# Optimization experiments

Hardware: AMD Instinct MI355X
Metric: run time of the kernel (lower is better)

## Reference

```python
import jax, jax.numpy as jnp
import numpy as np

N = 50000      # num nodes
E = 800000     # num edges (avg degree 16)
D = 128        # feature dim
HOP = 2        # number of propagation hops
FILL = 0.5     # self-loop fill value (A_hat = A + fill*I)


def setup_inputs() -> dict:
    key = jax.random.key(0)
    k1, k2, k3, k4, k5 = jax.random.split(key, 5)
    x_s = jax.random.normal(k1, (N, D), dtype=jnp.float32)
    x_t = jax.random.normal(k2, (N, D), dtype=jnp.float32)
    src = jax.random.randint(k3, (E,), 0, N)
    # guarantee no pre-existing self-loops so that appending all self-loops
    # exactly matches add_remaining_self_loops
    dst = (src + jax.random.randint(k4, (E,), 1, N)) % N
    edge_index = jnp.stack([src, dst]).astype(jnp.int32)
    edge_weight = jax.random.uniform(k5, (E,), dtype=jnp.float32)
    # DIMPA parameters, initialized to 1.0 per _reset_parameters
    w_s = jnp.ones((HOP + 1, 1), dtype=jnp.float32)
    w_t = jnp.ones((HOP + 1, 1), dtype=jnp.float32)
    return {"x_s": x_s, "x_t": x_t, "edge_index": edge_index,
            "edge_weight": edge_weight, "w_s": w_s, "w_t": w_t}


def _conv(x, row, col, w, n, fill):
    # Conv_Base: add self loops with weight `fill`, row-normalize by weighted
    # out-degree of `row`, scatter-add messages w_norm * x[row] onto `col`.
    loop = jnp.arange(n, dtype=row.dtype)
    row_a = jnp.concatenate([row, loop])
    col_a = jnp.concatenate([col, loop])
    w_a = jnp.concatenate([w, jnp.full((n,), fill, dtype=w.dtype)])
    deg = jax.ops.segment_sum(w_a, row_a, num_segments=n)
    deg_inv = jnp.where(deg == 0, jnp.zeros_like(deg), 1.0 / deg)  # inf -> 0
    w_norm = deg_inv[row_a] * w_a                                   # [E+n]
    return jax.ops.segment_sum(w_norm[:, None] * x[row_a], col_a, num_segments=n)


def reference(x_s, x_t, edge_index, edge_weight, w_s, w_t):
    n = x_s.shape[0]
    row, col = edge_index[0], edge_index[1]
    feat_s = w_s[0] * x_s
    feat_t = w_t[0] * x_t
    curr_s, curr_t = x_s, x_t
    for h in range(1, HOP + 1):
        curr_s = _conv(curr_s, row, col, edge_weight, n, FILL)
        # edge_index_t = edge_index[[1, 0]] -> swap row/col
        curr_t = _conv(curr_t, col, row, edge_weight, n, FILL)
        feat_s = feat_s + w_s[h] * curr_s
        feat_t = feat_t + w_t[h] * curr_t
    return jnp.concatenate([feat_s, feat_t], axis=1)  # [N, 2D]
```

## Files before the change

### kernel.cpp

```cpp
#include <hip/hip_runtime.h>

#define D 128
#define FILLV 0.5f
#define PAD 16
#define NXCD 8

typedef unsigned short u16;
typedef unsigned long long u64;

__device__ __forceinline__ u16 f2bf(float f) {
    unsigned u = __float_as_uint(f);
    u += 0x7FFF + ((u >> 16) & 1);
    return (u16)(u >> 16);
}
__device__ __forceinline__ float bf2f(u16 h) {
    return __uint_as_float(((unsigned)h) << 16);
}

__global__ void tobf_kernel(const float* __restrict__ x_s, const float* __restrict__ x_t,
                            u16* __restrict__ xb_s, u16* __restrict__ xb_t, long long nd) {
    long long t = (long long)blockIdx.x * blockDim.x + threadIdx.x;
    long long q = nd / 4;
    const float* x; u16* xb; long long i;
    if (t < q) { x = x_s; xb = xb_s; i = t * 4; }
    else if (t < 2 * q) { x = x_t; xb = xb_t; i = (t - q) * 4; }
    else return;
    float4 v = *(const float4*)(x + i);
    ushort4 o;
    o.x = f2bf(v.x); o.y = f2bf(v.y); o.z = f2bf(v.z); o.w = f2bf(v.w);
    *(ushort4*)(xb + i) = o;
}

__global__ void cnt_deg_kernel(const int* __restrict__ row, const int* __restrict__ col,
                               const float* __restrict__ w,
                               u64* __restrict__ cntp64, unsigned* __restrict__ ranks,
                               int E, int N) {
    int e = blockIdx.x * blockDim.x + threadIdx.x;
    if (e >= E) return;
    int r = row[e], c = col[e];
    unsigned fx = (unsigned)(w[e] * 16777216.0f);
    u64 add = (1ull << 32) | fx;
    u64 oc = atomicAdd(&cntp64[(size_t)c * (PAD / 2)], add);
    u64 orr = atomicAdd(&cntp64[(size_t)(N + r) * (PAD / 2)], add);
    unsigned pk = ((unsigned)(orr >> 32) << 16) | ((unsigned)(oc >> 32) & 0xffffu);
    __builtin_nontemporal_store(pk, ranks + e);
}

__global__ void invert_kernel(int* __restrict__ cntp, float* __restrict__ dinv, int total) {
    int i = blockIdx.x * blockDim.x + threadIdx.x;
    if (i >= total) return;
    u64 v = *(const u64*)&cntp[(size_t)i * PAD];
    float deg = (float)(unsigned)(v & 0xffffffffu) * (1.0f / 16777216.0f);
    dinv[i] = 1.0f / (deg + FILLV);
    cntp[(size_t)i * PAD] = (int)(v >> 32);
}

__global__ void scanA_kernel(const int* __restrict__ cntp, int* __restrict__ tsum, int total) {
    __shared__ int sh[256];
    int gid = blockIdx.x * 256 + threadIdx.x;
    sh[threadIdx.x] = (gid < total) ? cntp[(size_t)gid * PAD] : 0;
    __syncthreads();
    for (int off = 128; off > 0; off >>= 1) {
        if (threadIdx.x < off) sh[threadIdx.x] += sh[threadIdx.x + off];
        __syncthreads();
    }
    if (threadIdx.x == 0) tsum[blockIdx.x] = sh[0];
}

__global__ void scanB_kernel(const int* __restrict__ tsum, int* __restrict__ toff, int nt) {
    __shared__ int sh[512];
    int t = threadIdx.x;
    int v = (t < nt) ? tsum[t] : 0;
    sh[t] = v;
    __syncthreads();
    for (int off = 1; off < 512; off <<= 1) {
        int u = 0;
        if (t >= off) u = sh[t - off];
        __syncthreads();
        sh[t] += u;
        __syncthreads();
    }
    if (t < nt) toff[t] = sh[t] - v;
}

__global__ void scanC_kernel(const int* __restrict__ cntp, const int* __restrict__ toff,
                             int* __restrict__ start, int total, int grand_total) {
    __shared__ int sh[256];
    int gid = blockIdx.x * 256 + threadIdx.x;
    int v = (gid < total) ? cntp[(size_t)gid * PAD] : 0;
    sh[threadIdx.x] = v;
    __syncthreads();
    for (int off = 1; off < 256; off <<= 1) {
        int u = 0;
        if (threadIdx.x >= off) u = sh[threadIdx.x - off];
        __syncthreads();
        sh[threadIdx.x] += u;
        __syncthreads();
    }
    int run = toff[blockIdx.x] + sh[threadIdx.x] - v;
    if (gid < total) start[gid] = run;
    if (gid == 0) start[total] = grand_total;
}

__global__ void slot_kernel(const int* __restrict__ start,
                            const int* __restrict__ row, const int* __restrict__ col,
                            const float* __restrict__ w, const unsigned* __restrict__ ranks,
                            const float* __restrict__ dinv,
                            u64* __restrict__ ssst, u64* __restrict__ es, u64* __restrict__ et,
                            int E, int N) {
    int e = blockIdx.x * blockDim.x + threadIdx.x;
    if (e >= E) return;
    int r = row[e], c = col[e];
    float we = w[e];
    unsigned pk = __builtin_nontemporal_load(ranks + e);
    int ss = start[c] + (int)(pk & 0xffffu);
    int st = start[N + r] + (int)(pk >> 16);
    float wns = we * dinv[N + r];
    float wnt = we * dinv[c];
    u64 sv = ((u64)(unsigned)st << 32) | (unsigned)ss;
    u64 ev = ((u64)__float_as_uint(wns) << 32) | (unsigned)r;
    u64 tv = ((u64)__float_as_uint(wnt) << 32) | (unsigned)c;
    __builtin_nontemporal_store(sv, ssst + e);
    __builtin_nontemporal_store(ev, es + e);
    __builtin_nontemporal_store(tv, et + e);
}

__global__ void fillX_kernel(const u64* __restrict__ ssst,
                             const u64* __restrict__ es, const u64* __restrict__ et,
                             u64* __restrict__ edges, int E, int SL) {
    int e = (int)(blockIdx.x >> 3) * blockDim.x + threadIdx.x;
    int rid = blockIdx.x & 7;
    if (e >= E) return;
    int lo = rid * SL, hi = lo + SL;
    u64 sv = __builtin_nontemporal_load(ssst + e);
    int ss = (int)(unsigned)(sv & 0xffffffffu);
    int st = (int)(unsigned)(sv >> 32);
    bool ds = (ss >= lo) & (ss < hi);
    bool dt = (st >= lo) & (st < hi);
    if (ds) {
        u64 ev = __builtin_nontemporal_load(es + e);
        edges[ss] = ev;
    }
    if (dt) {
        u64 tv = __builtin_nontemporal_load(et + e);
        edges[st] = tv;
    }
}

__global__ void pull1_kernel(const int* __restrict__ start, const int2* __restrict__ edges,
                             const float* __restrict__ dinv,
                             const u16* __restrict__ xb_s, const u16* __restrict__ xb_t,
                             const float* __restrict__ x_s, const float* __restrict__ x_t,
                             u16* __restrict__ ab_s, u16* __restrict__ ab_t, int N) {
    int wid0 = (int)(((long long)blockIdx.x * blockDim.x + threadIdx.x) >> 6);
    int wid = __builtin_amdgcn_readfirstlane(wid0);
    int lane = threadIdx.x & 63;
    int half = lane >> 5, hl = lane & 31;
    if (wid >= 2 * N) return;
    const u16* xb; const float* x; u16* ab; int i, o;
    if (wid < N) { i = wid;     o = N; xb = xb_s; x = x_s; ab = ab_s; }
    else         { i = wid - N; o = 0; xb = xb_t; x = x_t; ab = ab_t; }
    int s0 = start[wid], s1 = start[wid + 1];
    float a0 = 0.f, a1 = 0.f, a2 = 0.f, a3 = 0.f;
    int k = s0;
    for (; k + 8 <= s1; k += 8) {
        int b = k + 4 * half;
        int2 p0 = edges[b], p1 = edges[b + 1], p2 = edges[b + 2], p3 = edges[b + 3];
        ushort4 v0 = *(const ushort4*)(xb + (size_t)p0.x * D + hl * 4);
        ushort4 v1 = *(const ushort4*)(xb + (size_t)p1.x * D + hl * 4);
        ushort4 v2 = *(const ushort4*)(xb + (size_t)p2.x * D + hl * 4);
        ushort4 v3 = *(const ushort4*)(xb + (size_t)p3.x * D + hl * 4);
        float w0v = __int_as_float(p0.y), w1v = __int_as_float(p1.y);
        float w2v = __int_as_float(p2.y), w3v = __int_as_float(p3.y);
        a0 += w0v * bf2f(v0.x) + w1v * bf2f(v1.x) + w2v * bf2f(v2.x) + w3v * bf2f(v3.x);
        a1 += w0v * bf2f(v0.y) + w1v * bf2f(v1.y) + w2v * bf2f(v2.y) + w3v * bf2f(v3.y);
        a2 += w0v * bf2f(v0.z) + w1v * bf2f(v1.z) + w2v * bf2f(v2.z) + w3v * bf2f(v3.z);
        a3 += w0v * bf2f(v0.w) + w1v * bf2f(v1.w) + w2v * bf2f(v2.w) + w3v * bf2f(v3.w);
    }
    if (k + 4 <= s1) {
        int b = k + 2 * half;
        int2 p0 = edges[b], p1 = edges[b + 1];
        ushort4 v0 = *(const ushort4*)(xb + (size_t)p0.x * D + hl * 4);
        ushort4 v1 = *(const ushort4*)(xb + (size_t)p1.x * D + hl * 4);
        float w0v = __int_as_float(p0.y), w1v = __int_as_float(p1.y);
        a0 += w0v * bf2f(v0.x) + w1v * bf2f(v1.x);
        a1 += w0v * bf2f(v0.y) + w1v * bf2f(v1.y);
        a2 += w0v * bf2f(v0.z) + w1v * bf2f(v1.z);
        a3 += w0v * bf2f(v0.w) + w1v * bf2f(v1.w);
        k += 4;
    }
    for (; k < s1; ++k) {
        if (half == 0) {
            int2 p = edges[k];
            ushort4 v = *(const ushort4*)(xb + (size_t)p.x * D + hl * 4);
            float wv = __int_as_float(p.y);
            a0 += wv * bf2f(v.x); a1 += wv * bf2f(v.y);
            a2 += wv * bf2f(v.z); a3 += wv * bf2f(v.w);
        }
    }
    a0 += __shfl_xor(a0, 32); a1 += __shfl_xor(a1, 32);
    a2 += __shfl_xor(a2, 32); a3 += __shfl_xor(a3, 32);
    if (half == 0) {
        float sw = FILLV * dinv[o + i];
        float4 xv = *(const float4*)(x + (size_t)i * D + hl * 4);
        a0 += sw * xv.x; a1 += sw * xv.y; a2 += sw * xv.z; a3 += sw * xv.w;
        ushort4 ov;
        ov.x = f2bf(a0); ov.y = f2bf(a1); ov.z = f2bf(a2); ov.w = f2bf(a3);
        *(ushort4*)(ab + (size_t)i * D + hl * 4) = ov;
    }
}

__global__ void pull2_kernel(const int* __restrict__ start, const int2* __restrict__ edges,
                             const float* __restrict__ dinv,
                             const u16* __restrict__ ab_s, const u16* __restrict__ ab_t,
                             const float* __restrict__ x_s, const float* __restrict__ x_t,
                             float* __restrict__ out,
                             const float* __restrict__ w_s, const float* __restrict__ w_t, int N) {
    int wid0 = (int)(((long long)blockIdx.x * blockDim.x + threadIdx.x) >> 6);
    int wid = __builtin_amdgcn_readfirstlane(wid0);
    int lane = threadIdx.x & 63;
    int half = lane >> 5, hl = lane & 31;
    if (wid >= 2 * N) return;
    const u16* ab; const float* x; const float* wv3; int i, o, hoff;
    if (wid < N) { i = wid;     o = N; ab = ab_s; x = x_s; wv3 = w_s; hoff = 0; }
    else         { i = wid - N; o = 0; ab = ab_t; x = x_t; wv3 = w_t; hoff = D; }
    int s0 = start[wid], s1 = start[wid + 1];
    float a0 = 0.f, a1 = 0.f, a2 = 0.f, a3 = 0.f;
    int k = s0;
    for (; k + 8 <= s1; k += 8) {
        int b = k + 4 * half;
        int2 p0 = edges[b], p1 = edges[b + 1], p2 = edges[b + 2], p3 = edges[b + 3];
        ushort4 v0 = *(const ushort4*)(ab + (size_t)p0.x * D + hl * 4);
        ushort4 v1 = *(const ushort4*)(ab + (size_t)p1.x * D + hl * 4);
        ushort4 v2 = *(const ushort4*)(ab + (size_t)p2.x * D + hl * 4);
        ushort4 v3 = *(const ushort4*)(ab + (size_t)p3.x * D + hl * 4);
        float w0v = __int_as_float(p0.y), w1v = __int_as_float(p1.y);
        float w2v = __int_as_float(p2.y), w3v = __int_as_float(p3.y);
        a0 += w0v * bf2f(v0.x) + w1v * bf2f(v1.x) + w2v * bf2f(v2.x) + w3v * bf2f(v3.x);
        a1 += w0v * bf2f(v0.y) + w1v * bf2f(v1.y) + w2v * bf2f(v2.y) + w3v * bf2f(v3.y);
        a2 += w0v * bf2f(v0.z) + w1v * bf2f(v1.z) + w2v * bf2f(v2.z) + w3v * bf2f(v3.z);
        a3 += w0v * bf2f(v0.w) + w1v * bf2f(v1.w) + w2v * bf2f(v2.w) + w3v * bf2f(v3.w);
    }
    if (k + 4 <= s1) {
        int b = k + 2 * half;
        int2 p0 = edges[b], p1 = edges[b + 1];
        ushort4 v0 = *(const ushort4*)(ab + (size_t)p0.x * D + hl * 4);
        ushort4 v1 = *(const ushort4*)(ab + (size_t)p1.x * D + hl * 4);
        float w0v = __int_as_float(p0.y), w1v = __int_as_float(p1.y);
        a0 += w0v * bf2f(v0.x) + w1v * bf2f(v1.x);
        a1 += w0v * bf2f(v0.y) + w1v * bf2f(v1.y);
        a2 += w0v * bf2f(v0.z) + w1v * bf2f(v1.z);
        a3 += w0v * bf2f(v0.w) + w1v * bf2f(v1.w);
        k += 4;
    }
    for (; k < s1; ++k) {
        if (half == 0) {
            int2 p = edges[k];
            ushort4 v = *(const ushort4*)(ab + (size_t)p.x * D + hl * 4);
            float wv = __int_as_float(p.y);
            a0 += wv * bf2f(v.x); a1 += wv * bf2f(v.y);
            a2 += wv * bf2f(v.z); a3 += wv * bf2f(v.w);
        }
    }
    a0 += __shfl_xor(a0, 32); a1 += __shfl_xor(a1, 32);
    a2 += __shfl_xor(a2, 32); a3 += __shfl_xor(a3, 32);
    if (half == 0) {
        float sw = FILLV * dinv[o + i];
        ushort4 av = *(const ushort4*)(ab + (size_t)i * D + hl * 4);
        float b0 = bf2f(av.x), b1 = bf2f(av.y), b2 = bf2f(av.z), b3 = bf2f(av.w);
        a0 += sw * b0; a1 += sw * b1; a2 += sw * b2; a3 += sw * b3;
        float w0 = wv3[0], w1 = wv3[1], w2 = wv3[2];
        float4 xv = *(const float4*)(x + (size_t)i * D + hl * 4);
        float4 ov;
        ov.x = w0 * xv.x + w1 * b0 + w2 * a0;
        ov.y = w0 * xv.y + w1 * b1 + w2 * a1;
        ov.z = w0 * xv.z + w1 * b2 + w2 * a2;
        ov.w = w0 * xv.w + w1 * b3 + w2 * a3;
        *(float4*)(out + (size_t)i * 2 * D + hoff + hl * 4) = ov;
    }
}

extern "C" void kernel_launch(void* const* d_in, const int* in_sizes, int n_in,
                              void* d_out, int out_size, void* d_ws, size_t ws_size,
                              hipStream_t stream) {
    const float* x_s = (const float*)d_in[0];
    const float* x_t = (const float*)d_in[1];
    const int*   ei  = (const int*)d_in[2];
    const float* ew  = (const float*)d_in[3];
    const float* w_s = (const float*)d_in[4];
    const float* w_t = (const float*)d_in[5];
    const int N = in_sizes[0] / D;
    const int E = in_sizes[3];
    const int* row = ei;
    const int* col = ei + E;

    const int total = 2 * N;
    const int nTiles = (total + 255) / 256;

    float* f      = (float*)d_ws;
    float* dinv   = f;
    int*   start  = (int*)(f + (size_t)total);
    int*   tsum   = start + (total + 2);
    int*   toff   = tsum + 512;
    char*  pc     = (char*)(toff + 512);
    pc = (char*)(((size_t)pc + 255) & ~(size_t)255);
    u64*   edges  = (u64*)pc;
    u16*   xb_s   = (u16*)(edges + 2 * (size_t)E);
    u16*   xb_t   = xb_s + (size_t)N * D;
    u16*   ab_s   = xb_t + (size_t)N * D;
    u16*   ab_t   = ab_s + (size_t)N * D;
    int*   cntp   = (int*)ab_s;

    unsigned* ranks = (unsigned*)d_out;
    char* po = (char*)d_out + (((size_t)E * 4 + 7) & ~(size_t)7);
    u64* ssst = (u64*)po;
    u64* es   = ssst + (size_t)E;
    u64* et   = es + (size_t)E;
    float* out = (float*)d_out;

    hipMemsetAsync(cntp, 0, (size_t)total * PAD * sizeof(int), stream);

    long long nd = (long long)N * D;
    int blkC  = (int)((nd / 2 + 255) / 256);
    int blkE  = (E + 255) / 256;
    int blk2N = (total + 255) / 256;
    tobf_kernel<<<blkC, 256, 0, stream>>>(x_s, x_t, xb_s, xb_t, nd);
    cnt_deg_kernel<<<blkE, 256, 0, stream>>>(row, col, ew, (u64*)cntp, ranks, E, N);
    invert_kernel<<<blk2N, 256, 0, stream>>>(cntp, dinv, total);
    scanA_kernel<<<nTiles, 256, 0, stream>>>(cntp, tsum, total);
    scanB_kernel<<<1, 512, 0, stream>>>(tsum, toff, nTiles);
    scanC_kernel<<<nTiles, 256, 0, stream>>>(cntp, toff, start, total, 2 * E);

    slot_kernel<<<blkE, 256, 0, stream>>>(start, row, col, ew, ranks, dinv,
                                          ssst, es, et, E, N);

    int SL = ((2 * E + NXCD - 1) / NXCD + 7) & ~7;
    fillX_kernel<<<NXCD * blkE, 256, 0, stream>>>(ssst, es, et, edges, E, SL);

    long long pull_threads = (long long)total * 64;
    int blkP = (int)((pull_threads + 255) / 256);
    pull1_kernel<<<blkP, 256, 0, stream>>>(start, (const int2*)edges, dinv, xb_s, xb_t,
                                           x_s, x_t, ab_s, ab_t, N);
    pull2_kernel<<<blkP, 256, 0, stream>>>(start, (const int2*)edges, dinv, ab_s, ab_t,
                                           x_s, x_t, out, w_s, w_t, N);
}
```

Before: 374.8 us.

## Fuse bf16 conversion with degree counting and merge invert into scan

```diff
diff --git a/kernel.cpp b/kernel.cpp
--- a/kernel.cpp
+++ b/kernel.cpp
@@ -2,7 +2,7 @@
 
 #define D 128
 #define FILLV 0.5f
-#define PAD 16
+#define PAD 2
 #define NXCD 8
 
 typedef unsigned short u16;
@@ -17,48 +17,49 @@
     return __uint_as_float(((unsigned)h) << 16);
 }
 
-__global__ void tobf_kernel(const float* __restrict__ x_s, const float* __restrict__ x_t,
-                            u16* __restrict__ xb_s, u16* __restrict__ xb_t, long long nd) {
-    long long t = (long long)blockIdx.x * blockDim.x + threadIdx.x;
-    long long q = nd / 4;
-    const float* x; u16* xb; long long i;
-    if (t < q) { x = x_s; xb = xb_s; i = t * 4; }
-    else if (t < 2 * q) { x = x_t; xb = xb_t; i = (t - q) * 4; }
-    else return;
-    float4 v = *(const float4*)(x + i);
-    ushort4 o;
-    o.x = f2bf(v.x); o.y = f2bf(v.y); o.z = f2bf(v.z); o.w = f2bf(v.w);
-    *(ushort4*)(xb + i) = o;
-}
-
-__global__ void cnt_deg_kernel(const int* __restrict__ row, const int* __restrict__ col,
-                               const float* __restrict__ w,
-                               u64* __restrict__ cntp64, unsigned* __restrict__ ranks,
-                               int E, int N) {
-    int e = blockIdx.x * blockDim.x + threadIdx.x;
-    if (e >= E) return;
-    int r = row[e], c = col[e];
-    unsigned fx = (unsigned)(w[e] * 16777216.0f);
-    u64 add = (1ull << 32) | fx;
-    u64 oc = atomicAdd(&cntp64[(size_t)c * (PAD / 2)], add);
-    u64 orr = atomicAdd(&cntp64[(size_t)(N + r) * (PAD / 2)], add);
-    unsigned pk = ((unsigned)(orr >> 32) << 16) | ((unsigned)(oc >> 32) & 0xffffu);
-    __builtin_nontemporal_store(pk, ranks + e);
-}
-
-__global__ void invert_kernel(int* __restrict__ cntp, float* __restrict__ dinv, int total) {
-    int i = blockIdx.x * blockDim.x + threadIdx.x;
-    if (i >= total) return;
-    u64 v = *(const u64*)&cntp[(size_t)i * PAD];
-    float deg = (float)(unsigned)(v & 0xffffffffu) * (1.0f / 16777216.0f);
-    dinv[i] = 1.0f / (deg + FILLV);
-    cntp[(size_t)i * PAD] = (int)(v >> 32);
-}
-
-__global__ void scanA_kernel(const int* __restrict__ cntp, int* __restrict__ tsum, int total) {
+__global__ void cnt_tobf_kernel(const int* __restrict__ row, const int* __restrict__ col,
+                                const float* __restrict__ w,
+                                u64* __restrict__ cntp64, unsigned* __restrict__ ranks,
+                                const float* __restrict__ x_s, const float* __restrict__ x_t,
+                                u16* __restrict__ xb_s, u16* __restrict__ xb_t,
+                                int E, int N, int blkE, long long nd) {
+    if ((int)blockIdx.x < blkE) {
+        int e = blockIdx.x * 256 + threadIdx.x;
+        if (e >= E) return;
+        int r = row[e], c = col[e];
+        unsigned fx = (unsigned)(w[e] * 16777216.0f);
+        u64 add = (1ull << 32) | fx;
+        u64 oc  = atomicAdd(&cntp64[(size_t)c], add);
+        u64 orr = atomicAdd(&cntp64[(size_t)N + r], add);
+        unsigned pk = ((unsigned)(orr >> 32) << 16) | ((unsigned)(oc >> 32) & 0xffffu);
+        __builtin_nontemporal_store(pk, ranks + e);
+    } else {
+        long long t = (long long)(blockIdx.x - blkE) * 256 + threadIdx.x;
+        long long q = nd / 4;
+        const float* x; u16* xb; long long i;
+        if (t < q) { x = x_s; xb = xb_s; i = t * 4; }
+        else if (t < 2 * q) { x = x_t; xb = xb_t; i = (t - q) * 4; }
+        else return;
+        float4 v = *(const float4*)(x + i);
+        ushort4 o;
+        o.x = f2bf(v.x); o.y = f2bf(v.y); o.z = f2bf(v.z); o.w = f2bf(v.w);
+        *(ushort4*)(xb + i) = o;
+    }
+}
+
+__global__ void scanAI_kernel(int* __restrict__ cntp, float* __restrict__ dinv,
+                              int* __restrict__ tsum, int total) {
     __shared__ int sh[256];
     int gid = blockIdx.x * 256 + threadIdx.x;
-    sh[threadIdx.x] = (gid < total) ? cntp[(size_t)gid * PAD] : 0;
+    int cnt = 0;
+    if (gid < total) {
+        u64 v = *(const u64*)&cntp[(size_t)gid * PAD];
+        float deg = (float)(unsigned)(v & 0xffffffffu) * (1.0f / 16777216.0f);
+        dinv[gid] = 1.0f / (deg + FILLV);
+        cnt = (int)(v >> 32);
+        cntp[(size_t)gid * PAD] = cnt;
+    }
+    sh[threadIdx.x] = cnt;
     __syncthreads();
     for (int off = 128; off > 0; off >>= 1) {
         if (threadIdx.x < off) sh[threadIdx.x] += sh[threadIdx.x + off];
@@ -323,11 +324,10 @@
     long long nd = (long long)N * D;
     int blkC  = (int)((nd / 2 + 255) / 256);
     int blkE  = (E + 255) / 256;
-    int blk2N = (total + 255) / 256;
-    tobf_kernel<<<blkC, 256, 0, stream>>>(x_s, x_t, xb_s, xb_t, nd);
-    cnt_deg_kernel<<<blkE, 256, 0, stream>>>(row, col, ew, (u64*)cntp, ranks, E, N);
-    invert_kernel<<<blk2N, 256, 0, stream>>>(cntp, dinv, total);
-    scanA_kernel<<<nTiles, 256, 0, stream>>>(cntp, tsum, total);
+    cnt_tobf_kernel<<<blkE + blkC, 256, 0, stream>>>(row, col, ew, (u64*)cntp, ranks,
+                                                     x_s, x_t, xb_s, xb_t,
+                                                     E, N, blkE, nd);
+    scanAI_kernel<<<nTiles, 256, 0, stream>>>(cntp, dinv, tsum, total);
     scanB_kernel<<<1, 512, 0, stream>>>(tsum, toff, nTiles);
     scanC_kernel<<<nTiles, 256, 0, stream>>>(cntp, toff, start, total, 2 * E);
 
```

After: 366.6 us. 2.2% less time.
